# Kernel optimization log

Hardware: AMD Instinct MI355X
Metric: run time of the kernel (lower is better)

The kernel has to match this reference:

```python
import jax, jax.numpy as jnp
import numpy as np

N, IN_C, E = 50000, 512, 800000
H, C = 2, 64          # heads, per-head channels
HC = H * C            # 128
OUT_C = 2
B = 64                # number of graphs
EPS = 1e-5
NEG_SLOPE = 0.2


def gat_conv(x, src, dst, W, a_src, a_dst, bias):
    """PyG GATConv (concat=True, add_self_loops already included in src/dst)."""
    n = x.shape[0]
    h = (x @ W).reshape(n, H, C)                      # [N,H,C]
    alpha_src = (h * a_src[None]).sum(-1)             # [N,H]
    alpha_dst = (h * a_dst[None]).sum(-1)             # [N,H]
    e = jax.nn.leaky_relu(alpha_src[src] + alpha_dst[dst], NEG_SLOPE)  # [E,H]
    # segment softmax over incoming edges of each destination node
    m = jax.ops.segment_max(e, dst, num_segments=n)   # [N,H]
    ex = jnp.exp(e - m[dst])
    denom = jax.ops.segment_sum(ex, dst, num_segments=n)
    alpha = ex / denom[dst]                           # [E,H]
    msg = h[src] * alpha[:, :, None]                  # [E,H,C]
    out = jax.ops.segment_sum(msg, dst, num_segments=n)  # [N,H,C]
    return out.reshape(n, HC) + bias


def batch_norm(x, gamma, beta):
    # BatchNorm1d in training mode: batch statistics over the node dim
    mu = x.mean(0)
    var = x.var(0)
    return gamma * (x - mu) * jax.lax.rsqrt(var + EPS) + beta


def setup_inputs() -> dict:
    key = jax.random.key(0)
    ks = jax.random.split(key, 16)
    x = jax.random.normal(ks[0], (N, IN_C), dtype=jnp.float32)
    edge_index = jax.random.randint(ks[1], (2, E), 0, N, dtype=jnp.int64)
    batch = jnp.sort(jax.random.randint(ks[2], (N,), 0, B, dtype=jnp.int64))
    g = lambda k, sh, fan: jax.random.normal(k, sh, dtype=jnp.float32) * (1.0 / np.sqrt(fan))
    return {
        "x": x, "edge_index": edge_index, "batch": batch,
        "W1": g(ks[3], (IN_C, HC), IN_C),
        "att_src1": g(ks[4], (H, C), C), "att_dst1": g(ks[5], (H, C), C),
        "b1": jnp.zeros((HC,), jnp.float32),
        "gamma1": jnp.ones((HC,), jnp.float32), "beta1": jnp.zeros((HC,), jnp.float32),
        "W2": g(ks[6], (HC, HC), HC),
        "att_src2": g(ks[7], (H, C), C), "att_dst2": g(ks[8], (H, C), C),
        "b2": jnp.zeros((HC,), jnp.float32),
        "gamma2": jnp.ones((HC,), jnp.float32), "beta2": jnp.zeros((HC,), jnp.float32),
        "Wlin": g(ks[9], (HC, OUT_C), HC),
        "blin": jnp.zeros((OUT_C,), jnp.float32),
    }


def reference(x, edge_index, batch, W1, att_src1, att_dst1, b1, gamma1, beta1,
              W2, att_src2, att_dst2, b2, gamma2, beta2, Wlin, blin):
    n = x.shape[0]
    # GATConv adds self-loops by default
    loop = jnp.arange(n, dtype=edge_index.dtype)
    src = jnp.concatenate([edge_index[0], loop])
    dst = jnp.concatenate([edge_index[1], loop])

    h = gat_conv(x, src, dst, W1, att_src1, att_dst1, b1)
    h = jax.nn.relu(batch_norm(h, gamma1, beta1))
    h = gat_conv(h, src, dst, W2, att_src2, att_dst2, b2)
    h = jax.nn.relu(batch_norm(h, gamma2, beta2))

    # global mean pool over graphs
    sums = jax.ops.segment_sum(h, batch, num_segments=B)           # [B,HC]
    cnt = jax.ops.segment_sum(jnp.ones((n,), h.dtype), batch, num_segments=B)
    pooled = sums / jnp.maximum(cnt, 1.0)[:, None]
    return pooled @ Wlin + blin                                    # [B,OUT_C]
```

## Files before the change

### kernel.cpp

```cpp
#include <hip/hip_runtime.h>
#include <hip/hip_bf16.h>
#include <cstdint>
#include <cstddef>

#define NN      50000
#define IN_C    512
#define EE      800000
#define ETOT    850000
#define HH      2
#define CC      64
#define HC      128
#define BB      64
#define OUTC    2
#define NEG_SLOPE 0.2f
#define BN_EPS  1e-5f

#define NBLK_SCAN ((NN + 255) / 256)

typedef __bf16 bf16x8 __attribute__((ext_vector_type(8)));
typedef float  f32x4  __attribute__((ext_vector_type(4)));

__device__ __forceinline__ unsigned f2bf(float f) {
    __bf16 b = (__bf16)f;
    return (unsigned)__builtin_bit_cast(unsigned short, b);
}

__device__ __forceinline__ void edge_sd(const int* __restrict__ ei, int e, int& s, int& d) {
    if (e < EE) { s = ei[e]; d = ei[EE + e]; }
    else        { s = e - EE; d = e - EE; }
}

__global__ __launch_bounds__(256) void deg_kernel(const int* __restrict__ ei, int* __restrict__ deg)
{
    int e = blockIdx.x * 256 + threadIdx.x;
    if (e >= ETOT) return;
    int d = (e < EE) ? ei[EE + e] : (e - EE);
    atomicAdd(&deg[d], 1);
}

__global__ __launch_bounds__(256) void bsum_kernel(const int* __restrict__ deg, int* __restrict__ bsum)
{
    int i = blockIdx.x * 256 + threadIdx.x;
    int v = (i < NN) ? deg[i] : 0;
    int lane = threadIdx.x & 63, wv = threadIdx.x >> 6;
#pragma unroll
    for (int o = 32; o > 0; o >>= 1) v += __shfl_down(v, o);
    __shared__ int ws[4];
    if (lane == 0) ws[wv] = v;
    __syncthreads();
    if (threadIdx.x == 0) bsum[blockIdx.x] = ws[0] + ws[1] + ws[2] + ws[3];
}

__global__ __launch_bounds__(256) void bscan_kernel(
    const int* __restrict__ bsum, int* __restrict__ bofs, int* __restrict__ rowp)
{
    int t = threadIdx.x;
    int lane = t & 63, wv = t >> 6;
    int v = (t < NBLK_SCAN) ? bsum[t] : 0;
    int x = v;
#pragma unroll
    for (int o = 1; o < 64; o <<= 1) {
        int y = __shfl_up(x, o);
        if (lane >= o) x += y;
    }
    __shared__ int ws[4];
    if (lane == 63) ws[wv] = x;
    __syncthreads();
    int wo = 0;
#pragma unroll
    for (int w = 0; w < 4; ++w) if (w < wv) wo += ws[w];
    if (t < NBLK_SCAN) bofs[t] = x + wo - v;
    if (t == 0) rowp[NN] = ETOT;
}

__global__ __launch_bounds__(256) void bapply_kernel(
    const int* __restrict__ deg, const int* __restrict__ bofs,
    int* __restrict__ rowp, int* __restrict__ cur)
{
    int i = blockIdx.x * 256 + threadIdx.x;
    int v = (i < NN) ? deg[i] : 0;
    int lane = threadIdx.x & 63, wv = threadIdx.x >> 6;
    int x = v;
#pragma unroll
    for (int o = 1; o < 64; o <<= 1) {
        int y = __shfl_up(x, o);
        if (lane >= o) x += y;
    }
    __shared__ int ws[4];
    if (lane == 63) ws[wv] = x;
    __syncthreads();
    int wo = 0;
#pragma unroll
    for (int w = 0; w < 4; ++w) if (w < wv) wo += ws[w];
    if (i < NN) {
        int r = bofs[blockIdx.x] + x + wo - v;
        rowp[i] = r; cur[i] = r;
    }
}

__global__ __launch_bounds__(256) void scatter_kernel(
    const int* __restrict__ ei, int* __restrict__ cur, int* __restrict__ esrc)
{
    int e = blockIdx.x * 256 + threadIdx.x;
    if (e >= ETOT) return;
    int s, d; edge_sd(ei, e, s, d);
    int pos = atomicAdd(&cur[d], 1);
    esrc[pos] = s;
}

__global__ __launch_bounds__(256) void wfrag_kernel(
    const float* __restrict__ W, unsigned short* __restrict__ Wf, int K)
{
    int t = blockIdx.x * 256 + threadIdx.x;
    if (t >= K * 16) return;
    int lane = t & 63, frag = t >> 6;
    int kblk = frag >> 3, nt = frag & 7;
    int quad = lane >> 4, ln = lane & 15;
    int kbase = kblk * 32 + quad * 8;
    int n = nt * 16 + ln;
    unsigned short u[8];
#pragma unroll
    for (int j = 0; j < 8; ++j)
        u[j] = (unsigned short)f2bf(W[(size_t)(kbase + j) * HC + n]);
    ushort4 a; a.x = u[0]; a.y = u[1]; a.z = u[2]; a.w = u[3];
    ushort4 b; b.x = u[4]; b.y = u[5]; b.z = u[6]; b.w = u[7];
    *(ushort4*)(Wf + (size_t)t * 8)     = a;
    *(ushort4*)(Wf + (size_t)t * 8 + 4) = b;
}

template<int K, bool AFFINE>
__global__ __launch_bounds__(256, 3) void mfma_gemm_kernel(
    const float* __restrict__ A, const unsigned short* __restrict__ Wf,
    const float* __restrict__ atts, const float* __restrict__ attd,
    unsigned* __restrict__ hb, float* __restrict__ as_, float* __restrict__ ad_,
    const float* __restrict__ sc, const float* __restrict__ sh)
{
    constexpr int NSTEP = K >> 5;
    constexpr int AD = (NSTEP < 4) ? NSTEP : 4;

    const int tid  = threadIdx.x;
    const int wave = tid >> 6, lane = tid & 63;
    const int quad = lane >> 4, ln = lane & 15;
    const int m0 = blockIdx.x * 64;
    const int myrow = m0 + wave * 16 + ln;
    const bool rok = (myrow < NN);
    const float* arow = A + (size_t)(rok ? myrow : 0) * K + quad * 8;
    const unsigned short* wbase = Wf + lane * 8;

    f32x4 acc[8];
#pragma unroll
    for (int nt = 0; nt < 8; ++nt) acc[nt] = (f32x4){0.f, 0.f, 0.f, 0.f};

    const float4 z4 = make_float4(0.f, 0.f, 0.f, 0.f);
    float4 pa[AD], pb[AD];
#pragma unroll
    for (int d = 0; d < AD; ++d) {
        if (rok) {
            pa[d] = *(const float4*)(arow + d * 32);
            pb[d] = *(const float4*)(arow + d * 32 + 4);
        } else { pa[d] = z4; pb[d] = z4; }
    }

    bf16x8 bfr[2][8];
#pragma unroll
    for (int nt = 0; nt < 8; ++nt) bfr[0][nt] = *(const bf16x8*)(wbase + nt * 512);

#pragma unroll
    for (int ks = 0; ks < NSTEP; ++ks) {
        const int cur = ks & 1;
        if (ks + 1 < NSTEP) {
            const unsigned short* wfp = wbase + (size_t)(ks + 1) * 4096;
#pragma unroll
            for (int nt = 0; nt < 8; ++nt)
                bfr[cur ^ 1][nt] = *(const bf16x8*)(wfp + nt * 512);
        }

        float4 ca = pa[ks % AD], cb = pb[ks % AD];
        float va[8] = {ca.x, ca.y, ca.z, ca.w, cb.x, cb.y, cb.z, cb.w};
        if (AFFINE) {
            const int kk = ks * 32 + quad * 8;
            const float4 s0 = *(const float4*)(sc + kk), s1 = *(const float4*)(sc + kk + 4);
            const float4 h0 = *(const float4*)(sh + kk), h1 = *(const float4*)(sh + kk + 4);
            va[0] = fmaxf(fmaf(s0.x, va[0], h0.x), 0.f);
            va[1] = fmaxf(fmaf(s0.y, va[1], h0.y), 0.f);
            va[2] = fmaxf(fmaf(s0.z, va[2], h0.z), 0.f);
            va[3] = fmaxf(fmaf(s0.w, va[3], h0.w), 0.f);
            va[4] = fmaxf(fmaf(s1.x, va[4], h1.x), 0.f);
            va[5] = fmaxf(fmaf(s1.y, va[5], h1.y), 0.f);
            va[6] = fmaxf(fmaf(s1.z, va[6], h1.z), 0.f);
            va[7] = fmaxf(fmaf(s1.w, va[7], h1.w), 0.f);
        }
        union { bf16x8 v; unsigned short u[8]; } af;
#pragma unroll
        for (int j = 0; j < 8; ++j) af.u[j] = (unsigned short)f2bf(va[j]);

        if (ks + AD < NSTEP && rok) {
            const float* nx = arow + (size_t)(ks + AD) * 32;
            pa[ks % AD] = *(const float4*)nx;
            pb[ks % AD] = *(const float4*)(nx + 4);
        }

#pragma unroll
        for (int nt = 0; nt < 8; ++nt)
            acc[nt] = __builtin_amdgcn_mfma_f32_16x16x32_bf16(af.v, bfr[cur][nt], acc[nt], 0, 0, 0);
    }

    float wsv[8], wdv[8];
#pragma unroll
    for (int nt = 0; nt < 8; ++nt) { wsv[nt] = atts[nt * 16 + ln]; wdv[nt] = attd[nt * 16 + ln]; }

    const int mbase = m0 + wave * 16 + quad * 4;
#pragma unroll
    for (int r = 0; r < 4; ++r) {
        int m = mbase + r;
        bool ok = (m < NN);
        float ps0 = 0.f, ps1 = 0.f, pd0 = 0.f, pd1 = 0.f;
#pragma unroll
        for (int nt = 0; nt < 8; ++nt) {
            float v = acc[nt][r];
            if (nt < 4) { ps0 = fmaf(v, wsv[nt], ps0); pd0 = fmaf(v, wdv[nt], pd0); }
            else        { ps1 = fmaf(v, wsv[nt], ps1); pd1 = fmaf(v, wdv[nt], pd1); }
        }
#pragma unroll
        for (int nt = 0; nt < 4; ++nt) {
            unsigned pk = f2bf(acc[nt][r]) | (f2bf(acc[nt + 4][r]) << 16);
            if (ok) hb[(size_t)m * 64 + nt * 16 + ln] = pk;
        }
#pragma unroll
        for (int o = 8; o > 0; o >>= 1) {
            ps0 += __shfl_down(ps0, o); ps1 += __shfl_down(ps1, o);
            pd0 += __shfl_down(pd0, o); pd1 += __shfl_down(pd1, o);
        }
        if (ok && ln == 0) {
            *(float2*)&as_[m * 2] = make_float2(ps0, ps1);
            *(float2*)&ad_[m * 2] = make_float2(pd0, pd1);
        }
    }
}

__global__ __launch_bounds__(256) void gat_agg_kernel(
    const int* __restrict__ rowp, const int* __restrict__ esrc,
    const float* __restrict__ as_, const float* __restrict__ ad_,
    const unsigned* __restrict__ hb, float* __restrict__ out)
{
    int node = (blockIdx.x * 256 + threadIdx.x) >> 6;
    int lane = threadIdx.x & 63;
    if (node >= NN) return;
    int beg = rowp[node], end = rowp[node + 1];
    float2 adv = *(const float2*)&ad_[node * 2];

    float l0 = 0.f, l1 = 0.f, a0 = 0.f, a1 = 0.f;

    for (int j0 = beg; j0 < end; j0 += 64) {
        int nj = min(64, end - j0);
        int   sl  = 0;
        float p0l = 0.f, p1l = 0.f;
        if (j0 + lane < end) {
            sl = esrc[j0 + lane];
            float2 t = *(const float2*)&as_[sl * 2];
            float e0 = t.x + adv.x; e0 = fmaxf(e0, NEG_SLOPE * e0);
            float e1 = t.y + adv.y; e1 = fmaxf(e1, NEG_SLOPE * e1);
            p0l = __expf(e0); p1l = __expf(e1);
        }
        l0 += p0l; l1 += p1l;

        int j = 0;
        for (; j + 2 <= nj; j += 2) {
            int sA = __shfl(sl, j), sB = __shfl(sl, j + 1);
            unsigned uA = hb[(size_t)sA * 64 + lane];
            unsigned uB = hb[(size_t)sB * 64 + lane];
            float pA0 = __shfl(p0l, j),     pA1 = __shfl(p1l, j);
            float pB0 = __shfl(p0l, j + 1), pB1 = __shfl(p1l, j + 1);
            a0 = fmaf(pA0, __uint_as_float(uA << 16), a0);
            a1 = fmaf(pA1, __uint_as_float(uA & 0xffff0000u), a1);
            a0 = fmaf(pB0, __uint_as_float(uB << 16), a0);
            a1 = fmaf(pB1, __uint_as_float(uB & 0xffff0000u), a1);
        }
        if (j < nj) {
            int s = __shfl(sl, j);
            unsigned u = hb[(size_t)s * 64 + lane];
            float p0 = __shfl(p0l, j), p1 = __shfl(p1l, j);
            a0 = fmaf(p0, __uint_as_float(u << 16), a0);
            a1 = fmaf(p1, __uint_as_float(u & 0xffff0000u), a1);
        }
    }

#pragma unroll
    for (int o = 1; o < 64; o <<= 1) {
        l0 += __shfl_xor(l0, o); l1 += __shfl_xor(l1, o);
    }
    out[(size_t)node * HC + lane]      = a0 / l0;
    out[(size_t)node * HC + 64 + lane] = a1 / l1;
}

__global__ __launch_bounds__(256) void bn_stats_kernel(
    const float* __restrict__ x, float* __restrict__ stats)
{
    int c = threadIdx.x & 127;
    int half = threadIdx.x >> 7;
    float s = 0.f, sq = 0.f;
    for (int r = blockIdx.x * 2 + half; r < NN; r += gridDim.x * 2) {
        float v = x[(size_t)r * HC + c];
        s += v; sq += v * v;
    }
    __shared__ float ls[256], lq[256];
    ls[threadIdx.x] = s; lq[threadIdx.x] = sq;
    __syncthreads();
    if (half == 0) {
        s += ls[threadIdx.x + 128];
        sq += lq[threadIdx.x + 128];
        atomicAdd(&stats[c], s);
        atomicAdd(&stats[128 + c], sq);
    }
}

__global__ void bn_params_kernel(
    const float* __restrict__ stats, const float* __restrict__ gamma,
    const float* __restrict__ beta, float* __restrict__ sc, float* __restrict__ sh)
{
    int c = threadIdx.x;
    const float inv_n = 1.0f / (float)NN;
    float mu = stats[c] * inv_n;
    float var = stats[128 + c] * inv_n - mu * mu;
    float rs = rsqrtf(var + BN_EPS);
    float s = gamma[c] * rs;
    sc[c] = s;
    sh[c] = beta[c] - mu * s;
}

__global__ __launch_bounds__(256) void pool_kernel(
    const float* __restrict__ x, const float* __restrict__ sc,
    const float* __restrict__ sh, const int* __restrict__ batch,
    float* __restrict__ pool, float* __restrict__ cnt)
{
    int c = threadIdx.x & 127;
    int half = threadIdx.x >> 7;
    int r0 = blockIdx.x * 64;
    int rend = min(r0 + 64, NN);
    float s = sc[c], b = sh[c];
    int cur = -1; float acc = 0.f, ccount = 0.f;
    for (int r = r0 + half; r < rend; r += 2) {
        int g = batch[r];
        if (g != cur) {
            if (cur >= 0) {
                atomicAdd(&pool[cur * HC + c], acc);
                if (c == 0) atomicAdd(&cnt[cur], ccount);
            }
            cur = g; acc = 0.f; ccount = 0.f;
        }
        float v = x[(size_t)r * HC + c];
        acc += fmaxf(fmaf(s, v, b), 0.f);
        ccount += 1.f;
    }
    if (cur >= 0) {
        atomicAdd(&pool[cur * HC + c], acc);
        if (c == 0) atomicAdd(&cnt[cur], ccount);
    }
}

__global__ void final_kernel(
    const float* __restrict__ pool, const float* __restrict__ cnt,
    const float* __restrict__ Wlin, const float* __restrict__ blin,
    float* __restrict__ outp)
{
    int t = threadIdx.x;
    int b = t >> 1, oc = t & 1;
    float inv = 1.f / fmaxf(cnt[b], 1.f);
    float s = blin[oc];
    for (int c = 0; c < HC; ++c)
        s += pool[b * HC + c] * inv * Wlin[c * 2 + oc];
    outp[b * 2 + oc] = s;
}

static constexpr size_t OFF_OUT   = 0;
static constexpr size_t OFF_AS    = OFF_OUT + (size_t)NN*HC;
static constexpr size_t OFF_AD    = OFF_AS  + (size_t)NN*HH;
static constexpr size_t OFF_ST1   = OFF_AD  + (size_t)NN*HH;
static constexpr size_t OFF_ST2   = OFF_ST1 + 256;
static constexpr size_t OFF_SC1   = OFF_ST2 + 256;
static constexpr size_t OFF_SH1   = OFF_SC1 + 128;
static constexpr size_t OFF_SC2   = OFF_SH1 + 128;
static constexpr size_t OFF_SH2   = OFF_SC2 + 128;
static constexpr size_t OFF_POOL  = OFF_SH2 + 128;
static constexpr size_t OFF_CNT   = OFF_POOL+ (size_t)BB*HC;
static constexpr size_t OFF_ZEND  = OFF_CNT + BB;
static constexpr size_t IOFF_DEG  = 0;
static constexpr size_t IOFF_ROWP = IOFF_DEG  + NN;
static constexpr size_t IOFF_CUR  = IOFF_ROWP + NN + 1;
static constexpr size_t IOFF_BSUM = IOFF_CUR  + NN;
static constexpr size_t IOFF_BOFS = IOFF_BSUM + NBLK_SCAN;
static constexpr size_t IOFF_ESRC = IOFF_BOFS + NBLK_SCAN;
static constexpr size_t IOFF_HB   = (IOFF_ESRC + ETOT + 3) & ~(size_t)3;
static constexpr size_t IOFF_WF1  = IOFF_HB + (size_t)NN*64;
static constexpr size_t IOFF_WF2  = IOFF_WF1 + (size_t)IN_C*64;
static constexpr size_t IOFF_END  = IOFF_WF2 + (size_t)HC*64;

extern "C" void kernel_launch(void* const* d_in, const int* in_sizes, int n_in,
                              void* d_out, int out_size, void* d_ws, size_t ws_size,
                              hipStream_t stream)
{
    const float* x       = (const float*)d_in[0];
    const int*   ei      = (const int*)  d_in[1];
    const int*   batch   = (const int*)  d_in[2];
    const float* W1      = (const float*)d_in[3];
    const float* atts1   = (const float*)d_in[4];
    const float* attd1   = (const float*)d_in[5];
    const float* gamma1  = (const float*)d_in[7];
    const float* beta1   = (const float*)d_in[8];
    const float* W2      = (const float*)d_in[9];
    const float* atts2   = (const float*)d_in[10];
    const float* attd2   = (const float*)d_in[11];
    const float* gamma2  = (const float*)d_in[13];
    const float* beta2   = (const float*)d_in[14];
    const float* Wlin    = (const float*)d_in[15];
    const float* blin    = (const float*)d_in[16];
    float* outp = (float*)d_out;

    float* ws    = (float*)d_ws;
    float* out   = ws + OFF_OUT;
    float* as_   = ws + OFF_AS;
    float* ad_   = ws + OFF_AD;
    float* st1   = ws + OFF_ST1;
    float* st2   = ws + OFF_ST2;
    float* sc1   = ws + OFF_SC1;
    float* sh1   = ws + OFF_SH1;
    float* sc2   = ws + OFF_SC2;
    float* sh2   = ws + OFF_SH2;
    float* pool  = ws + OFF_POOL;
    float* cnt   = ws + OFF_CNT;

    int* iws  = (int*)(ws + OFF_ZEND);
    int* deg  = iws + IOFF_DEG;
    int* rowp = iws + IOFF_ROWP;
    int* curp = iws + IOFF_CUR;
    int* bsum = iws + IOFF_BSUM;
    int* bofs = iws + IOFF_BOFS;
    int* esrc = iws + IOFF_ESRC;
    unsigned* hb = (unsigned*)(iws + IOFF_HB);
    unsigned short* Wf1 = (unsigned short*)(iws + IOFF_WF1);
    unsigned short* Wf2 = (unsigned short*)(iws + IOFF_WF2);

    const int EDGE_BLK  = (ETOT + 255) / 256;
    const int GEMM_BLK  = (NN + 63) / 64;
    const int WAVE_BLK  = (NN + 3) / 4;
    const int POOL_BLK  = (NN + 63) / 64;

    hipMemsetAsync(st1, 0, (OFF_ZEND - OFF_ST1) * sizeof(float), stream);
    hipMemsetAsync(deg, 0, NN * sizeof(int), stream);

    wfrag_kernel<<<(IN_C * 16 + 255) / 256, 256, 0, stream>>>(W1, Wf1, IN_C);
    wfrag_kernel<<<(HC   * 16 + 255) / 256, 256, 0, stream>>>(W2, Wf2, HC);
    deg_kernel<<<EDGE_BLK, 256, 0, stream>>>(ei, deg);
    bsum_kernel<<<NBLK_SCAN, 256, 0, stream>>>(deg, bsum);
    bscan_kernel<<<1, 256, 0, stream>>>(bsum, bofs, rowp);
    bapply_kernel<<<NBLK_SCAN, 256, 0, stream>>>(deg, bofs, rowp, curp);
    scatter_kernel<<<EDGE_BLK, 256, 0, stream>>>(ei, curp, esrc);

    mfma_gemm_kernel<IN_C, false><<<GEMM_BLK, 256, 0, stream>>>(
        x, Wf1, atts1, attd1, hb, as_, ad_, nullptr, nullptr);
    gat_agg_kernel<<<WAVE_BLK, 256, 0, stream>>>(rowp, esrc, as_, ad_, hb, out);
    bn_stats_kernel<<<512, 256, 0, stream>>>(out, st1);
    bn_params_kernel<<<1, 128, 0, stream>>>(st1, gamma1, beta1, sc1, sh1);

    mfma_gemm_kernel<HC, true><<<GEMM_BLK, 256, 0, stream>>>(
        out, Wf2, atts2, attd2, hb, as_, ad_, sc1, sh1);
    gat_agg_kernel<<<WAVE_BLK, 256, 0, stream>>>(rowp, esrc, as_, ad_, hb, out);
    bn_stats_kernel<<<512, 256, 0, stream>>>(out, st2);
    bn_params_kernel<<<1, 128, 0, stream>>>(st2, gamma2, beta2, sc2, sh2);

    pool_kernel<<<POOL_BLK, 256, 0, stream>>>(out, sc2, sh2, batch, pool, cnt);
    final_kernel<<<1, 128, 0, stream>>>(pool, cnt, Wlin, blin, outp);
}
```

Measured before the change: 488.2 us.

## Partition edge atomics by XCD range and split GEMM output columns across blocks

The degree count and CSR scatter now launch blocks that map to XCDs by blockIdx, and each block only does atomics for destinations in its XCD's node range. The aim is to keep atomic traffic local to one XCD's L2, at the cost of every edge index being read eight times. The GEMM now splits the 128 output columns into two halves handled by separate blocks. This halves per-thread accumulators and B fragments to help occupancy, but the A rows are loaded twice. The hb layout is changed to match, and the aggregation kernel now has each lane handle one head with an adjusted output channel mapping.

```diff
diff --git a/kernel.cpp b/kernel.cpp
--- a/kernel.cpp
+++ b/kernel.cpp
@@ -17,6 +17,11 @@
 
 #define NBLK_SCAN ((NN + 255) / 256)
 
+#define NXCD     8
+#define NPX      ((NN + NXCD - 1) / NXCD)
+#define EDGES_PER_SLOT 2048
+#define NSLOT    ((ETOT + EDGES_PER_SLOT - 1) / EDGES_PER_SLOT)
+
 typedef __bf16 bf16x8 __attribute__((ext_vector_type(8)));
 typedef float  f32x4  __attribute__((ext_vector_type(4)));
 
@@ -25,17 +30,20 @@
     return (unsigned)__builtin_bit_cast(unsigned short, b);
 }
 
-__device__ __forceinline__ void edge_sd(const int* __restrict__ ei, int e, int& s, int& d) {
-    if (e < EE) { s = ei[e]; d = ei[EE + e]; }
-    else        { s = e - EE; d = e - EE; }
-}
-
 __global__ __launch_bounds__(256) void deg_kernel(const int* __restrict__ ei, int* __restrict__ deg)
 {
-    int e = blockIdx.x * 256 + threadIdx.x;
-    if (e >= ETOT) return;
-    int d = (e < EE) ? ei[EE + e] : (e - EE);
-    atomicAdd(&deg[d], 1);
+    const int xcd  = blockIdx.x & (NXCD - 1);
+    const int slot = blockIdx.x >> 3;
+    const int lo = xcd * NPX, hi = lo + NPX;
+    const int base = slot * EDGES_PER_SLOT;
+#pragma unroll
+    for (int it = 0; it < EDGES_PER_SLOT / 256; ++it) {
+        int e = base + it * 256 + threadIdx.x;
+        if (e < ETOT) {
+            int d = (e < EE) ? ei[EE + e] : (e - EE);
+            if (d >= lo && d < hi) atomicAdd(&deg[d], 1);
+        }
+    }
 }
 
 __global__ __launch_bounds__(256) void bsum_kernel(const int* __restrict__ deg, int* __restrict__ bsum)
@@ -101,11 +109,23 @@
 __global__ __launch_bounds__(256) void scatter_kernel(
     const int* __restrict__ ei, int* __restrict__ cur, int* __restrict__ esrc)
 {
-    int e = blockIdx.x * 256 + threadIdx.x;
-    if (e >= ETOT) return;
-    int s, d; edge_sd(ei, e, s, d);
-    int pos = atomicAdd(&cur[d], 1);
-    esrc[pos] = s;
+    const int xcd  = blockIdx.x & (NXCD - 1);
+    const int slot = blockIdx.x >> 3;
+    const int lo = xcd * NPX, hi = lo + NPX;
+    const int base = slot * EDGES_PER_SLOT;
+#pragma unroll
+    for (int it = 0; it < EDGES_PER_SLOT / 256; ++it) {
+        int e = base + it * 256 + threadIdx.x;
+        if (e < ETOT) {
+            int s, d;
+            if (e < EE) { s = ei[e]; d = ei[EE + e]; }
+            else        { s = e - EE; d = s; }
+            if (d >= lo && d < hi) {
+                int pos = atomicAdd(&cur[d], 1);
+                esrc[pos] = s;
+            }
+        }
+    }
 }
 
 __global__ __launch_bounds__(256) void wfrag_kernel(
@@ -129,7 +149,7 @@
 }
 
 template<int K, bool AFFINE>
-__global__ __launch_bounds__(256, 3) void mfma_gemm_kernel(
+__global__ __launch_bounds__(256) void mfma_gemm_kernel(
     const float* __restrict__ A, const unsigned short* __restrict__ Wf,
     const float* __restrict__ atts, const float* __restrict__ attd,
     unsigned* __restrict__ hb, float* __restrict__ as_, float* __restrict__ ad_,
@@ -141,15 +161,17 @@
     const int tid  = threadIdx.x;
     const int wave = tid >> 6, lane = tid & 63;
     const int quad = lane >> 4, ln = lane & 15;
-    const int m0 = blockIdx.x * 64;
+    const int tilei = blockIdx.x >> 1;
+    const int half  = blockIdx.x & 1;
+    const int m0 = tilei * 64;
     const int myrow = m0 + wave * 16 + ln;
     const bool rok = (myrow < NN);
     const float* arow = A + (size_t)(rok ? myrow : 0) * K + quad * 8;
-    const unsigned short* wbase = Wf + lane * 8;
-
-    f32x4 acc[8];
-#pragma unroll
-    for (int nt = 0; nt < 8; ++nt) acc[nt] = (f32x4){0.f, 0.f, 0.f, 0.f};
+    const unsigned short* wbase = Wf + (size_t)(half * 4) * 512 + lane * 8;
+
+    f32x4 acc[4];
+#pragma unroll
+    for (int nt = 0; nt < 4; ++nt) acc[nt] = (f32x4){0.f, 0.f, 0.f, 0.f};
 
     const float4 z4 = make_float4(0.f, 0.f, 0.f, 0.f);
     float4 pa[AD], pb[AD];
@@ -161,9 +183,9 @@
         } else { pa[d] = z4; pb[d] = z4; }
     }
 
-    bf16x8 bfr[2][8];
-#pragma unroll
-    for (int nt = 0; nt < 8; ++nt) bfr[0][nt] = *(const bf16x8*)(wbase + nt * 512);
+    bf16x8 bfr[2][4];
+#pragma unroll
+    for (int nt = 0; nt < 4; ++nt) bfr[0][nt] = *(const bf16x8*)(wbase + nt * 512);
 
 #pragma unroll
     for (int ks = 0; ks < NSTEP; ++ks) {
@@ -171,7 +193,7 @@
         if (ks + 1 < NSTEP) {
             const unsigned short* wfp = wbase + (size_t)(ks + 1) * 4096;
 #pragma unroll
-            for (int nt = 0; nt < 8; ++nt)
+            for (int nt = 0; nt < 4; ++nt)
                 bfr[cur ^ 1][nt] = *(const bf16x8*)(wfp + nt * 512);
         }
 
@@ -201,39 +223,43 @@
         }
 
 #pragma unroll
-        for (int nt = 0; nt < 8; ++nt)
+        for (int nt = 0; nt < 4; ++nt)
             acc[nt] = __builtin_amdgcn_mfma_f32_16x16x32_bf16(af.v, bfr[cur][nt], acc[nt], 0, 0, 0);
     }
 
-    float wsv[8], wdv[8];
-#pragma unroll
-    for (int nt = 0; nt < 8; ++nt) { wsv[nt] = atts[nt * 16 + ln]; wdv[nt] = attd[nt * 16 + ln]; }
+    float wsv[4], wdv[4];
+#pragma unroll
+    for (int nt = 0; nt < 4; ++nt) {
+        wsv[nt] = atts[(half * 4 + nt) * 16 + ln];
+        wdv[nt] = attd[(half * 4 + nt) * 16 + ln];
+    }
 
     const int mbase = m0 + wave * 16 + quad * 4;
 #pragma unroll
     for (int r = 0; r < 4; ++r) {
         int m = mbase + r;
         bool ok = (m < NN);
-        float ps0 = 0.f, ps1 = 0.f, pd0 = 0.f, pd1 = 0.f;
-#pragma unroll
-        for (int nt = 0; nt < 8; ++nt) {
+        float ps = 0.f, pd = 0.f;
+#pragma unroll
+        for (int nt = 0; nt < 4; ++nt) {
             float v = acc[nt][r];
-            if (nt < 4) { ps0 = fmaf(v, wsv[nt], ps0); pd0 = fmaf(v, wdv[nt], pd0); }
-            else        { ps1 = fmaf(v, wsv[nt], ps1); pd1 = fmaf(v, wdv[nt], pd1); }
-        }
-#pragma unroll
-        for (int nt = 0; nt < 4; ++nt) {
-            unsigned pk = f2bf(acc[nt][r]) | (f2bf(acc[nt + 4][r]) << 16);
-            if (ok) hb[(size_t)m * 64 + nt * 16 + ln] = pk;
+            ps = fmaf(v, wsv[nt], ps);
+            pd = fmaf(v, wdv[nt], pd);
+        }
+        unsigned u0 = f2bf(acc[0][r]) | (f2bf(acc[1][r]) << 16);
+        unsigned u1 = f2bf(acc[2][r]) | (f2bf(acc[3][r]) << 16);
+        if (ok) {
+            hb[(size_t)m * 64 + half * 32 + ln]      = u0;
+            hb[(size_t)m * 64 + half * 32 + 16 + ln] = u1;
         }
 #pragma unroll
         for (int o = 8; o > 0; o >>= 1) {
-            ps0 += __shfl_down(ps0, o); ps1 += __shfl_down(ps1, o);
-            pd0 += __shfl_down(pd0, o); pd1 += __shfl_down(pd1, o);
+            ps += __shfl_down(ps, o);
+            pd += __shfl_down(pd, o);
         }
         if (ok && ln == 0) {
-            *(float2*)&as_[m * 2] = make_float2(ps0, ps1);
-            *(float2*)&ad_[m * 2] = make_float2(pd0, pd1);
+            as_[m * 2 + half] = ps;
+            ad_[m * 2 + half] = pd;
         }
     }
 }
@@ -248,8 +274,10 @@
     if (node >= NN) return;
     int beg = rowp[node], end = rowp[node + 1];
     float2 adv = *(const float2*)&ad_[node * 2];
-
-    float l0 = 0.f, l1 = 0.f, a0 = 0.f, a1 = 0.f;
+    const bool h1 = (lane >= 32);
+    const int c_lo = lane + (lane & 48);
+
+    float l0 = 0.f, l1 = 0.f, a_lo = 0.f, a_hi = 0.f;
 
     for (int j0 = beg; j0 < end; j0 += 64) {
         int nj = min(64, end - j0);
@@ -271,17 +299,20 @@
             unsigned uB = hb[(size_t)sB * 64 + lane];
             float pA0 = __shfl(p0l, j),     pA1 = __shfl(p1l, j);
             float pB0 = __shfl(p0l, j + 1), pB1 = __shfl(p1l, j + 1);
-            a0 = fmaf(pA0, __uint_as_float(uA << 16), a0);
-            a1 = fmaf(pA1, __uint_as_float(uA & 0xffff0000u), a1);
-            a0 = fmaf(pB0, __uint_as_float(uB << 16), a0);
-            a1 = fmaf(pB1, __uint_as_float(uB & 0xffff0000u), a1);
+            float pA = h1 ? pA1 : pA0;
+            float pB = h1 ? pB1 : pB0;
+            a_lo = fmaf(pA, __uint_as_float(uA << 16), a_lo);
+            a_hi = fmaf(pA, __uint_as_float(uA & 0xffff0000u), a_hi);
+            a_lo = fmaf(pB, __uint_as_float(uB << 16), a_lo);
+            a_hi = fmaf(pB, __uint_as_float(uB & 0xffff0000u), a_hi);
         }
         if (j < nj) {
             int s = __shfl(sl, j);
             unsigned u = hb[(size_t)s * 64 + lane];
             float p0 = __shfl(p0l, j), p1 = __shfl(p1l, j);
-            a0 = fmaf(p0, __uint_as_float(u << 16), a0);
-            a1 = fmaf(p1, __uint_as_float(u & 0xffff0000u), a1);
+            float p = h1 ? p1 : p0;
+            a_lo = fmaf(p, __uint_as_float(u << 16), a_lo);
+            a_hi = fmaf(p, __uint_as_float(u & 0xffff0000u), a_hi);
         }
     }
 
@@ -289,8 +320,9 @@
     for (int o = 1; o < 64; o <<= 1) {
         l0 += __shfl_xor(l0, o); l1 += __shfl_xor(l1, o);
     }
-    out[(size_t)node * HC + lane]      = a0 / l0;
-    out[(size_t)node * HC + 64 + lane] = a1 / l1;
+    float rl = 1.f / (h1 ? l1 : l0);
+    out[(size_t)node * HC + c_lo]      = a_lo * rl;
+    out[(size_t)node * HC + c_lo + 16] = a_hi * rl;
 }
 
 __global__ __launch_bounds__(256) void bn_stats_kernel(
@@ -440,8 +472,8 @@
     unsigned short* Wf1 = (unsigned short*)(iws + IOFF_WF1);
     unsigned short* Wf2 = (unsigned short*)(iws + IOFF_WF2);
 
-    const int EDGE_BLK  = (ETOT + 255) / 256;
-    const int GEMM_BLK  = (NN + 63) / 64;
+    const int BIN_BLK   = NXCD * NSLOT;
+    const int GEMM_BLK  = 2 * ((NN + 63) / 64);
     const int WAVE_BLK  = (NN + 3) / 4;
     const int POOL_BLK  = (NN + 63) / 64;
 
@@ -450,11 +482,11 @@
 
     wfrag_kernel<<<(IN_C * 16 + 255) / 256, 256, 0, stream>>>(W1, Wf1, IN_C);
     wfrag_kernel<<<(HC   * 16 + 255) / 256, 256, 0, stream>>>(W2, Wf2, HC);
-    deg_kernel<<<EDGE_BLK, 256, 0, stream>>>(ei, deg);
+    deg_kernel<<<BIN_BLK, 256, 0, stream>>>(ei, deg);
     bsum_kernel<<<NBLK_SCAN, 256, 0, stream>>>(deg, bsum);
     bscan_kernel<<<1, 256, 0, stream>>>(bsum, bofs, rowp);
     bapply_kernel<<<NBLK_SCAN, 256, 0, stream>>>(deg, bofs, rowp, curp);
-    scatter_kernel<<<EDGE_BLK, 256, 0, stream>>>(ei, curp, esrc);
+    scatter_kernel<<<BIN_BLK, 256, 0, stream>>>(ei, curp, esrc);
 
     mfma_gemm_kernel<IN_C, false><<<GEMM_BLK, 256, 0, stream>>>(
         x, Wf1, atts1, attd1, hb, as_, ad_, nullptr, nullptr);
```

After: 487.4 us. No clear change (-0.2%).
